# Kernel optimization log

Hardware: AMD Instinct MI355X
Metric: run time of the kernel (lower is better)

## Reference

```python
import jax, jax.numpy as jnp
import numpy as np

EPS = 1e-12

def _dot(x, y):
    return jnp.sum(x * y, axis=-1)

def _safe(x):
    # avoid div-by-zero for degenerate triangles / unused where-branches
    return jnp.where(jnp.abs(x) < EPS, EPS, x)

def _closest_point_on_tri(p, a, b, c):
    """Ericson real-time-collision-detection closest point on triangle.
    p: [B,Q,1,3]; a,b,c: [B,1,F,3]. Returns [B,Q,F,3]."""
    ab = b - a
    ac = c - a
    ap = p - a
    d1 = _dot(ab, ap)
    d2 = _dot(ac, ap)
    bp = p - b
    d3 = _dot(ab, bp)
    d4 = _dot(ac, bp)
    cp = p - c
    d5 = _dot(ab, cp)
    d6 = _dot(ac, cp)
    vc = d1 * d4 - d3 * d2
    vb = d5 * d2 - d1 * d6
    va = d3 * d6 - d5 * d4
    # candidate points (all computed densely, selected by masks)
    t_ab = (d1 / _safe(d1 - d3))[..., None]
    t_ac = (d2 / _safe(d2 - d6))[..., None]
    t_bc = ((d4 - d3) / _safe((d4 - d3) + (d5 - d6)))[..., None]
    denom = _safe(va + vb + vc)
    v = (vb / denom)[..., None]
    w = (vc / denom)[..., None]
    res = a + ab * v + ac * w  # face interior
    cond_bc = ((va <= 0) & ((d4 - d3) >= 0) & ((d5 - d6) >= 0))[..., None]
    cond_ac = ((vb <= 0) & (d2 >= 0) & (d6 <= 0))[..., None]
    cond_c = ((d6 >= 0) & (d5 <= d6))[..., None]
    cond_ab = ((vc <= 0) & (d1 >= 0) & (d3 <= 0))[..., None]
    cond_b = ((d3 >= 0) & (d4 <= d3))[..., None]
    cond_a = ((d1 <= 0) & (d2 <= 0))[..., None]
    res = jnp.where(cond_bc, b + (c - b) * t_bc, res)
    res = jnp.where(cond_ac, a + ac * t_ac, res)
    res = jnp.where(cond_c, c, res)
    res = jnp.where(cond_ab, a + ab * t_ab, res)
    res = jnp.where(cond_b, b, res)
    res = jnp.where(cond_a, a, res)
    return res

def setup_inputs() -> dict:
    key = jax.random.key(0)
    k1, k2, k3 = jax.random.split(key, 3)
    B, nQ, nV, nF = 1, 8192, 1024, 2048
    vertices = jax.random.normal(k1, (B, nV, 3), dtype=jnp.float32)
    query = jax.random.normal(k2, (B, nQ, 3), dtype=jnp.float32)
    faces = jax.random.randint(k3, (nF, 3), 0, nV, dtype=jnp.int32)
    return {"faces": faces, "vertices": vertices, "query": query}

def reference(faces, vertices, query):
    # gather triangle vertices: [B, F, 3(verts), 3(xyz)]
    tri = vertices[:, faces, :]
    a = tri[:, :, 0][:, None]  # [B,1,F,3]
    b = tri[:, :, 1][:, None]
    c = tri[:, :, 2][:, None]
    p = query[:, :, None, :]   # [B,Q,1,3]
    cp = _closest_point_on_tri(p, a, b, c)        # [B,Q,F,3]
    d2 = jnp.sum((p - cp) ** 2, axis=-1)          # [B,Q,F]
    idx = jnp.argmin(d2, axis=-1)                 # [B,Q]
    B_, Q_ = idx.shape
    cp_best = jnp.take_along_axis(
        cp, jnp.broadcast_to(idx[:, :, None, None], (B_, Q_, 1, 3)), axis=2
    )[:, :, 0]                                    # [B,Q,3]
    d2_best = jnp.take_along_axis(d2, idx[:, :, None], axis=2)[:, :, 0]
    # face normals for sign (outside if along normal), per-face then gathered
    n = jnp.cross(tri[:, :, 1] - tri[:, :, 0], tri[:, :, 2] - tri[:, :, 0])  # [B,F,3]
    n_best = jnp.take_along_axis(n, jnp.broadcast_to(idx[:, :, None], (B_, Q_, 3)) % n.shape[1] * 0 + idx[:, :, None], axis=1)  # [B,Q,3]
    sign = jnp.where(jnp.sum((query - cp_best) * n_best, axis=-1) >= 0, 1.0, -1.0)
    sdist = sign * jnp.sqrt(jnp.maximum(d2_best, 0.0))
    phi = jnp.concatenate([cp_best, sdist[..., None]], axis=-1)  # [B,Q,4]
    return phi
```

## Files before the change

### kernel.cpp

```cpp
#include <hip/hip_runtime.h>
#include <stdint.h>


__device__ __forceinline__ float safe32(float x) {
    return (fabsf(x) < 1e-12f) ? 1e-12f : x;
}

__device__ __forceinline__ float closest_point32(
    float px, float py, float pz,
    float ax, float ay, float az,
    float bx, float by, float bz,
    float cx, float cy, float cz,
    float& rx, float& ry, float& rz)
{
#pragma clang fp contract(off)
    float abx = bx - ax, aby = by - ay, abz = bz - az;
    float acx = cx - ax, acy = cy - ay, acz = cz - az;
    float cbx = cx - bx, cby = cy - by, cbz = cz - bz;

    float apx = px - ax, apy = py - ay, apz = pz - az;
    float bpx = px - bx, bpy = py - by, bpz = pz - bz;
    float qpx = px - cx, qpy = py - cy, qpz = pz - cz;

    float d1 = ((abx * apx) + (aby * apy)) + (abz * apz);
    float d2 = ((acx * apx) + (acy * apy)) + (acz * apz);
    float d3 = ((abx * bpx) + (aby * bpy)) + (abz * bpz);
    float d4 = ((acx * bpx) + (acy * bpy)) + (acz * bpz);
    float d5 = ((abx * qpx) + (aby * qpy)) + (abz * qpz);
    float d6 = ((acx * qpx) + (acy * qpy)) + (acz * qpz);

    float vc = (d1 * d4) - (d3 * d2);
    float vb = (d5 * d2) - (d1 * d6);
    float va = (d3 * d6) - (d5 * d4);
    float e1 = d4 - d3;
    float e2 = d5 - d6;

    bool ca  = (d1 <= 0.0f) && (d2 <= 0.0f);
    bool cb2 = (d3 >= 0.0f) && (d4 <= d3);
    bool cab = (vc <= 0.0f) && (d1 >= 0.0f) && (d3 <= 0.0f);
    bool cc  = (d6 >= 0.0f) && (d5 <= d6);
    bool cac = (vb <= 0.0f) && (d2 >= 0.0f) && (d6 <= 0.0f);
    bool cbc = (va <= 0.0f) && (e1 >= 0.0f) && (e2 >= 0.0f);

    int region = 6;
    if (cbc) region = 5;
    if (cac) region = 4;
    if (cc)  region = 3;
    if (cab) region = 2;
    if (cb2) region = 1;
    if (ca)  region = 0;

    float denom = safe32((va + vb) + vc);

    float num1 = 0.0f, den1 = 1.0f;
    if (region == 2) { num1 = d1; den1 = safe32(d1 - d3); }
    if (region == 4) { num1 = d2; den1 = safe32(d2 - d6); }
    if (region == 5) { num1 = e1; den1 = safe32(e1 + e2); }
    if (region == 6) { num1 = vb; den1 = denom; }
    float num2 = (region == 6) ? vc : 0.0f;
    float q1 = num1 / den1;
    float q2 = num2 / denom;

    float basx = ax, basy = ay, basz = az;
    if (region == 1 || region == 5) { basx = bx; basy = by; basz = bz; }
    if (region == 3)                { basx = cx; basy = cy; basz = cz; }

    float t1x = 0.0f, t1y = 0.0f, t1z = 0.0f;
    if (region == 2 || region == 6) { t1x = abx; t1y = aby; t1z = abz; }
    if (region == 4)                { t1x = acx; t1y = acy; t1z = acz; }
    if (region == 5)                { t1x = cbx; t1y = cby; t1z = cbz; }

    float t2x = (region == 6) ? acx : 0.0f;
    float t2y = (region == 6) ? acy : 0.0f;
    float t2z = (region == 6) ? acz : 0.0f;

    rx = (basx + (t1x * q1)) + (t2x * q2);
    ry = (basy + (t1y * q1)) + (t2y * q2);
    rz = (basz + (t1z * q1)) + (t2z * q2);

    float dx = px - rx, dy = py - ry, dz = pz - rz;
    return ((dx * dx) + (dy * dy)) + (dz * dz);
}

__global__ void k_prep(const int* __restrict__ faces, const float* __restrict__ verts,
                       float* __restrict__ tris, int nF)
{
    int i = blockIdx.x * 256 + threadIdx.x;
    if (i < nF) {
        int i0 = faces[i * 3 + 0], i1 = faces[i * 3 + 1], i2 = faces[i * 3 + 2];
        float* t = &tris[i * 9];
        t[0] = verts[i0 * 3]; t[1] = verts[i0 * 3 + 1]; t[2] = verts[i0 * 3 + 2];
        t[3] = verts[i1 * 3]; t[4] = verts[i1 * 3 + 1]; t[5] = verts[i1 * 3 + 2];
        t[6] = verts[i2 * 3]; t[7] = verts[i2 * 3 + 1]; t[8] = verts[i2 * 3 + 2];
    }
}

__global__ __launch_bounds__(256) void k_main(
    const float* __restrict__ tris, const float* __restrict__ query,
    float* __restrict__ out, int nF, int nQ)
{
#pragma clang fp contract(off)
    const int gtid = blockIdx.x * 256 + threadIdx.x;
    const int q = gtid >> 6;
    const int lane = threadIdx.x & 63;
    if (q >= nQ) return;

    const float px = query[q * 3];
    const float py = query[q * 3 + 1];
    const float pz = query[q * 3 + 2];

    float best = 3.402823466e38f;
    int bidx = 0x7fffffff;
    for (int f = lane; f < nF; f += 64) {
        const float* t = &tris[f * 9];
        float rx, ry, rz;
        float d2 = closest_point32(px, py, pz,
            t[0], t[1], t[2], t[3], t[4], t[5], t[6], t[7], t[8],
            rx, ry, rz);
        if (d2 < best) { best = d2; bidx = f; }
    }

    for (int off = 32; off > 0; off >>= 1) {
        float od = __shfl_down(best, off);
        int   oi = __shfl_down(bidx, off);
        if (od < best || (od == best && oi < bidx)) { best = od; bidx = oi; }
    }

    if (lane == 0) {
        const float* t = &tris[bidx * 9];
        float ax = t[0], ay = t[1], az = t[2];
        float bx = t[3], by = t[4], bz = t[5];
        float cx = t[6], cy = t[7], cz = t[8];

        float rx, ry, rz;
        closest_point32(px, py, pz, ax, ay, az, bx, by, bz, cx, cy, cz,
                        rx, ry, rz);

        float abx = bx - ax, aby = by - ay, abz = bz - az;
        float acx = cx - ax, acy = cy - ay, acz = cz - az;
        float nx = (aby * acz) - (abz * acy);
        float ny = (abz * acx) - (abx * acz);
        float nz = (abx * acy) - (aby * acx);

        float dx = px - rx, dy = py - ry, dz = pz - rz;
        float sdot = ((dx * nx) + (dy * ny)) + (dz * nz);
        float sgn = (sdot >= 0.0f) ? 1.0f : -1.0f;
        float sdist = sgn * __fsqrt_rn(fmaxf(best, 0.0f));

        out[q * 4 + 0] = rx;
        out[q * 4 + 1] = ry;
        out[q * 4 + 2] = rz;
        out[q * 4 + 3] = sdist;
    }
}

extern "C" void kernel_launch(void* const* d_in, const int* in_sizes, int n_in,
                              void* d_out, int out_size, void* d_ws, size_t ws_size,
                              hipStream_t stream) {
    const int* faces = (const int*)d_in[0];
    const float* verts = (const float*)d_in[1];
    const float* query = (const float*)d_in[2];
    float* out = (float*)d_out;

    const int nF = in_sizes[0] / 3;
    const int nQ = in_sizes[2] / 3;

    float* tris = (float*)d_ws;

    k_prep<<<(nF + 255) / 256, 256, 0, stream>>>(faces, verts, tris, nF);

    int blocks = (nQ * 64 + 255) / 256;
    k_main<<<blocks, 256, 0, stream>>>(tris, query, out, nF, nQ);
}
```

Measured before the change: 132.4 us.

## Tile faces in shared memory, one thread per query, atomic 64-bit min reduction

Restructures the search so each thread owns one query and each block loops over a chunk of 64 faces staged in LDS. Results are combined across face-chunks with a packed (distance, index) 64-bit atomicMin, and a separate finalize kernel computes the output. The prep kernel now precomputes edge vectors into 20-float records so they are not recomputed per query-face pair. Region selection becomes branch-free. This removes per-wave redundant global loads and the per-query shuffle reduction, at the cost of global atomics, an extra kernel launch and key initialization.

```diff
diff --git a/kernel.cpp b/kernel.cpp
--- a/kernel.cpp
+++ b/kernel.cpp
@@ -1,22 +1,26 @@
 #include <hip/hip_runtime.h>
 #include <stdint.h>
 
+
+#define QPB 256
+#define FC  64
+#define RECF 20
 
 __device__ __forceinline__ float safe32(float x) {
     return (fabsf(x) < 1e-12f) ? 1e-12f : x;
 }
 
-__device__ __forceinline__ float closest_point32(
-    float px, float py, float pz,
-    float ax, float ay, float az,
-    float bx, float by, float bz,
-    float cx, float cy, float cz,
+__device__ __forceinline__ float cp32(
+    float px, float py, float pz, const float4* __restrict__ rec,
     float& rx, float& ry, float& rz)
 {
 #pragma clang fp contract(off)
-    float abx = bx - ax, aby = by - ay, abz = bz - az;
-    float acx = cx - ax, acy = cy - ay, acz = cz - az;
-    float cbx = cx - bx, cby = cy - by, cbz = cz - bz;
+    float4 r0 = rec[0], r1 = rec[1], r2 = rec[2], r3 = rec[3], r4 = rec[4];
+    float ax = r0.x, ay = r0.y, az = r0.z, bx = r0.w;
+    float by = r1.x, bz = r1.y, cx = r1.z, cy = r1.w;
+    float cz = r2.x, abx = r2.y, aby = r2.z, abz = r2.w;
+    float acx = r3.x, acy = r3.y, acz = r3.z, cbx = r3.w;
+    float cby = r4.x, cbz = r4.y;
 
     float apx = px - ax, apy = py - ay, apz = pz - az;
     float bpx = px - bx, bpy = py - by, bpz = pz - bz;
@@ -36,43 +40,43 @@
     float e2 = d5 - d6;
 
     bool ca  = (d1 <= 0.0f) && (d2 <= 0.0f);
-    bool cb2 = (d3 >= 0.0f) && (d4 <= d3);
+    bool cb_ = (d3 >= 0.0f) && (d4 <= d3);
     bool cab = (vc <= 0.0f) && (d1 >= 0.0f) && (d3 <= 0.0f);
     bool cc  = (d6 >= 0.0f) && (d5 <= d6);
     bool cac = (vb <= 0.0f) && (d2 >= 0.0f) && (d6 <= 0.0f);
     bool cbc = (va <= 0.0f) && (e1 >= 0.0f) && (e2 >= 0.0f);
 
-    int region = 6;
-    if (cbc) region = 5;
-    if (cac) region = 4;
-    if (cc)  region = 3;
-    if (cab) region = 2;
-    if (cb2) region = 1;
-    if (ca)  region = 0;
+    bool tk  = ca;
+    bool m_b  = cb_ && !tk;  tk = tk || cb_;
+    bool m_ab = cab && !tk;  tk = tk || cab;
+    bool m_c  = cc  && !tk;  tk = tk || cc;
+    bool m_ac = cac && !tk;  tk = tk || cac;
+    bool m_bc = cbc && !tk;  tk = tk || cbc;
+    bool m_in = !tk;
 
-    float denom = safe32((va + vb) + vc);
-
-    float num1 = 0.0f, den1 = 1.0f;
-    if (region == 2) { num1 = d1; den1 = safe32(d1 - d3); }
-    if (region == 4) { num1 = d2; den1 = safe32(d2 - d6); }
-    if (region == 5) { num1 = e1; den1 = safe32(e1 + e2); }
-    if (region == 6) { num1 = vb; den1 = denom; }
-    float num2 = (region == 6) ? vc : 0.0f;
+    float denom_raw = (va + vb) + vc;
+    float num1 = m_ab ? d1 : m_ac ? d2 : m_bc ? e1 : m_in ? vb : 0.0f;
+    float den1_raw = m_ab ? (d1 - d3) : m_ac ? (d2 - d6)
+                   : m_bc ? (e1 + e2) : m_in ? denom_raw : 1.0f;
+    float den1  = safe32(den1_raw);
+    float denom = safe32(denom_raw);
+    float num2  = m_in ? vc : 0.0f;
     float q1 = num1 / den1;
     float q2 = num2 / denom;
 
-    float basx = ax, basy = ay, basz = az;
-    if (region == 1 || region == 5) { basx = bx; basy = by; basz = bz; }
-    if (region == 3)                { basx = cx; basy = cy; basz = cz; }
+    bool sel_b = m_b || m_bc;
+    float basx = m_c ? cx : sel_b ? bx : ax;
+    float basy = m_c ? cy : sel_b ? by : ay;
+    float basz = m_c ? cz : sel_b ? bz : az;
 
-    float t1x = 0.0f, t1y = 0.0f, t1z = 0.0f;
-    if (region == 2 || region == 6) { t1x = abx; t1y = aby; t1z = abz; }
-    if (region == 4)                { t1x = acx; t1y = acy; t1z = acz; }
-    if (region == 5)                { t1x = cbx; t1y = cby; t1z = cbz; }
+    bool s_ab = m_ab || m_in;
+    float t1x = m_bc ? cbx : m_ac ? acx : s_ab ? abx : 0.0f;
+    float t1y = m_bc ? cby : m_ac ? acy : s_ab ? aby : 0.0f;
+    float t1z = m_bc ? cbz : m_ac ? acz : s_ab ? abz : 0.0f;
 
-    float t2x = (region == 6) ? acx : 0.0f;
-    float t2y = (region == 6) ? acy : 0.0f;
-    float t2z = (region == 6) ? acz : 0.0f;
+    float t2x = m_in ? acx : 0.0f;
+    float t2y = m_in ? acy : 0.0f;
+    float t2z = m_in ? acz : 0.0f;
 
     rx = (basx + (t1x * q1)) + (t2x * q2);
     ry = (basy + (t1y * q1)) + (t2y * q2);
@@ -83,75 +87,91 @@
 }
 
 __global__ void k_prep(const int* __restrict__ faces, const float* __restrict__ verts,
-                       float* __restrict__ tris, int nF)
+                       float* __restrict__ tris, unsigned long long* __restrict__ keys,
+                       int nF, int nQ)
 {
+#pragma clang fp contract(off)
     int i = blockIdx.x * 256 + threadIdx.x;
+    if (i < nQ) keys[i] = 0xffffffffffffffffULL;
     if (i < nF) {
         int i0 = faces[i * 3 + 0], i1 = faces[i * 3 + 1], i2 = faces[i * 3 + 2];
-        float* t = &tris[i * 9];
-        t[0] = verts[i0 * 3]; t[1] = verts[i0 * 3 + 1]; t[2] = verts[i0 * 3 + 2];
-        t[3] = verts[i1 * 3]; t[4] = verts[i1 * 3 + 1]; t[5] = verts[i1 * 3 + 2];
-        t[6] = verts[i2 * 3]; t[7] = verts[i2 * 3 + 1]; t[8] = verts[i2 * 3 + 2];
+        float ax = verts[i0 * 3], ay = verts[i0 * 3 + 1], az = verts[i0 * 3 + 2];
+        float bx = verts[i1 * 3], by = verts[i1 * 3 + 1], bz = verts[i1 * 3 + 2];
+        float cx = verts[i2 * 3], cy = verts[i2 * 3 + 1], cz = verts[i2 * 3 + 2];
+        float* t = &tris[i * RECF];
+        t[0]  = ax; t[1]  = ay; t[2]  = az; t[3]  = bx;
+        t[4]  = by; t[5]  = bz; t[6]  = cx; t[7]  = cy;
+        t[8]  = cz;
+        t[9]  = bx - ax; t[10] = by - ay; t[11] = bz - az;
+        t[12] = cx - ax; t[13] = cy - ay; t[14] = cz - az;
+        t[15] = cx - bx; t[16] = cy - by; t[17] = cz - bz;
+        t[18] = 0.0f; t[19] = 0.0f;
     }
 }
 
-__global__ __launch_bounds__(256) void k_main(
+__global__ __launch_bounds__(QPB) void k_main(
     const float* __restrict__ tris, const float* __restrict__ query,
-    float* __restrict__ out, int nF, int nQ)
+    unsigned long long* __restrict__ keys, int nF, int nQ)
 {
-#pragma clang fp contract(off)
-    const int gtid = blockIdx.x * 256 + threadIdx.x;
-    const int q = gtid >> 6;
-    const int lane = threadIdx.x & 63;
+    __shared__ float4 s4[FC * (RECF / 4)];
+    const int fbase = blockIdx.y * FC;
+    const int nf = min(FC, nF - fbase);
+    const int tid = threadIdx.x;
+
+    {
+        const float4* src = (const float4*)&tris[(size_t)fbase * RECF];
+        for (int i = tid; i < nf * (RECF / 4); i += QPB) s4[i] = src[i];
+    }
+    __syncthreads();
+
+    const int q = blockIdx.x * QPB + tid;
     if (q >= nQ) return;
-
-    const float px = query[q * 3];
-    const float py = query[q * 3 + 1];
-    const float pz = query[q * 3 + 2];
+    const float px = query[q * 3], py = query[q * 3 + 1], pz = query[q * 3 + 2];
 
     float best = 3.402823466e38f;
     int bidx = 0x7fffffff;
-    for (int f = lane; f < nF; f += 64) {
-        const float* t = &tris[f * 9];
+    for (int f = 0; f < nf; ++f) {
         float rx, ry, rz;
-        float d2 = closest_point32(px, py, pz,
-            t[0], t[1], t[2], t[3], t[4], t[5], t[6], t[7], t[8],
-            rx, ry, rz);
-        if (d2 < best) { best = d2; bidx = f; }
+        float d2 = cp32(px, py, pz, &s4[f * (RECF / 4)], rx, ry, rz);
+        if (d2 < best) { best = d2; bidx = fbase + f; }
     }
+    unsigned long long key =
+        ((unsigned long long)__float_as_uint(best) << 32) | (unsigned)bidx;
+    atomicMin(&keys[q], key);
+}
 
-    for (int off = 32; off > 0; off >>= 1) {
-        float od = __shfl_down(best, off);
-        int   oi = __shfl_down(bidx, off);
-        if (od < best || (od == best && oi < bidx)) { best = od; bidx = oi; }
-    }
+__global__ void k_final(const float* __restrict__ tris, const float* __restrict__ query,
+                        const unsigned long long* __restrict__ keys,
+                        float* __restrict__ out, int nQ)
+{
+#pragma clang fp contract(off)
+    int q = blockIdx.x * 256 + threadIdx.x;
+    if (q >= nQ) return;
+    unsigned long long key = keys[q];
+    unsigned idx = (unsigned)(key & 0xffffffffu);
+    float best_d2 = __uint_as_float((unsigned)(key >> 32));
 
-    if (lane == 0) {
-        const float* t = &tris[bidx * 9];
-        float ax = t[0], ay = t[1], az = t[2];
-        float bx = t[3], by = t[4], bz = t[5];
-        float cx = t[6], cy = t[7], cz = t[8];
+    const float px = query[q * 3], py = query[q * 3 + 1], pz = query[q * 3 + 2];
+    const float4* rec = (const float4*)&tris[(size_t)idx * RECF];
+    float rx, ry, rz;
+    cp32(px, py, pz, rec, rx, ry, rz);
 
-        float rx, ry, rz;
-        closest_point32(px, py, pz, ax, ay, az, bx, by, bz, cx, cy, cz,
-                        rx, ry, rz);
+    float4 r2 = rec[2], r3 = rec[3];
+    float abx = r2.y, aby = r2.z, abz = r2.w;
+    float acx = r3.x, acy = r3.y, acz = r3.z;
+    float nx = (aby * acz) - (abz * acy);
+    float ny = (abz * acx) - (abx * acz);
+    float nz = (abx * acy) - (aby * acx);
 
-        float abx = bx - ax, aby = by - ay, abz = bz - az;
-        float acx = cx - ax, acy = cy - ay, acz = cz - az;
-        float nx = (aby * acz) - (abz * acy);
-        float ny = (abz * acx) - (abx * acz);
-        float nz = (abx * acy) - (aby * acx);
+    float dx = px - rx, dy = py - ry, dz = pz - rz;
+    float sdot = ((dx * nx) + (dy * ny)) + (dz * nz);
+    float sgn = (sdot >= 0.0f) ? 1.0f : -1.0f;
+    float sdist = sgn * __fsqrt_rn(fmaxf(best_d2, 0.0f));
 
-        float dx = px - rx, dy = py - ry, dz = pz - rz;
-        float sdot = ((dx * nx) + (dy * ny)) + (dz * nz);
-        float sgn = (sdot >= 0.0f) ? 1.0f : -1.0f;
-        float sdist = sgn * __fsqrt_rn(fmaxf(best, 0.0f));
-
-        out[q * 4 + 0] = rx;
-        out[q * 4 + 1] = ry;
-        out[q * 4 + 2] = rz;
-        out[q * 4 + 3] = sdist;
-    }
+    out[q * 4 + 0] = rx;
+    out[q * 4 + 1] = ry;
+    out[q * 4 + 2] = rz;
+    out[q * 4 + 3] = sdist;
 }
 
 extern "C" void kernel_launch(void* const* d_in, const int* in_sizes, int n_in,
@@ -165,10 +185,14 @@
     const int nF = in_sizes[0] / 3;
     const int nQ = in_sizes[2] / 3;
 
-    float* tris = (float*)d_ws;
+    unsigned long long* keys = (unsigned long long*)d_ws;
+    float* tris = (float*)((char*)d_ws + (size_t)nQ * 8);
 
-    k_prep<<<(nF + 255) / 256, 256, 0, stream>>>(faces, verts, tris, nF);
+    int prep_threads = (nQ > nF ? nQ : nF);
+    k_prep<<<(prep_threads + 255) / 256, 256, 0, stream>>>(faces, verts, tris, keys, nF, nQ);
 
-    int blocks = (nQ * 64 + 255) / 256;
-    k_main<<<blocks, 256, 0, stream>>>(tris, query, out, nF, nQ);
+    dim3 grid((nQ + QPB - 1) / QPB, (nF + FC - 1) / FC);
+    k_main<<<grid, QPB, 0, stream>>>(tris, query, keys, nF, nQ);
+
+    k_final<<<(nQ + 255) / 256, 256, 0, stream>>>(tris, query, keys, out, nQ);
 }
```

Measured after the change: 127.2 us. 4.0% less time.
